# Kernel tuning notes

Measured on AMD Instinct MI355X. Metric: run time of the kernel, lower is better.

Reference implementation:

```python
import jax, jax.numpy as jnp
import numpy as np

BS, S, DIM, H = 4, 2048, 1024, 16
DH = DIM // H  # 64


def setup_inputs() -> dict:
    key = jax.random.key(0)
    ks = jax.random.split(key, 12)
    def lin(k, fan_in):
        bound = 1.0 / np.sqrt(fan_in)
        kw, kb = jax.random.split(k)
        W = jax.random.uniform(kw, (DIM, DIM), jnp.float32, -bound, bound)
        b = jax.random.uniform(kb, (DIM,), jnp.float32, -bound, bound)
        return W, b
    Wq, bq = lin(ks[0], DIM)
    Wk, bk = lin(ks[1], DIM)
    Wv, bv = lin(ks[2], DIM)
    Wo, bo = lin(ks[3], DIM)
    return {
        "query": jax.random.normal(ks[4], (BS, S, DIM), jnp.float32),
        "key": jax.random.normal(ks[5], (BS, S, DIM), jnp.float32),
        "value": jax.random.normal(ks[6], (BS, S, DIM), jnp.float32),
        "mask": jnp.ones((BS, S), jnp.int32),
        "Wq": Wq, "bq": bq, "Wk": Wk, "bk": bk,
        "Wv": Wv, "bv": bv, "Wo": Wo, "bo": bo,
    }


def reference(query, key, value, mask, Wq, bq, Wk, bk, Wv, bv, Wo, bo):
    bs, q_len, dim = query.shape
    def shape_heads(x):  # (bs, s, dim) -> (bs, H, s, DH)
        return x.reshape(bs, -1, H, DH).transpose(0, 2, 1, 3)
    # Linear projections (torch Linear: x @ W.T + b)
    q = shape_heads(query @ Wq.T + bq)
    k = shape_heads(key @ Wk.T + bk)
    v = shape_heads(value @ Wv.T + bv)
    q = q / jnp.sqrt(jnp.asarray(DH, q.dtype))
    # scores: (bs, H, q_len, k_len)
    scores = jnp.einsum('bhqd,bhkd->bhqk', q, k)
    neg = jnp.asarray(-jnp.inf, scores.dtype)
    pad = (mask == 0)[:, None, None, :]  # (bs,1,1,k_len)
    scores = jnp.where(pad, neg, scores)
    weights = jax.nn.softmax(scores, axis=-1)
    # dropout is identity in eval mode (reference is deterministic)
    context = jnp.einsum('bhqk,bhkd->bhqd', weights, v)
    context = context.transpose(0, 2, 1, 3).reshape(bs, q_len, dim)
    return context @ Wo.T + bo
```

## Files before the change

kernel.cpp:

```cpp
#include <hip/hip_runtime.h>
#include <hip/hip_bf16.h>
#include <math.h>

#define BSZ 4
#define SEQ 2048
#define DIMN 1024
#define NHEAD 16
#define DHEAD 64
#define MROWS (BSZ*SEQ)

typedef __bf16 bf16x8 __attribute__((ext_vector_type(8)));
typedef float  f32x4  __attribute__((ext_vector_type(4)));
typedef float  f32x16 __attribute__((ext_vector_type(16)));
typedef float  fvec4  __attribute__((ext_vector_type(4)));
typedef short  s16x4  __attribute__((ext_vector_type(4)));
typedef short  s16x8  __attribute__((ext_vector_type(8)));

__device__ __forceinline__ short f2bf(float v) {
  __hip_bfloat16 b = __float2bfloat16(v);
  return *reinterpret_cast<short*>(&b);
}
__device__ __forceinline__ float bf2f(short s) {
  __hip_bfloat16 b = *reinterpret_cast<__hip_bfloat16*>(&s);
  return __bfloat162float(b);
}

__device__ __forceinline__ void gld_lds16(const void* g, void* l) {
  __builtin_amdgcn_global_load_lds((const __attribute__((address_space(1))) void*)g,
                                   (__attribute__((address_space(3))) void*)l, 16, 0, 0);
}

#define QSC 0.18033688011112042f

__global__ __launch_bounds__(256) void pack_w4(
    const float* __restrict__ Wq, const float* __restrict__ Wk,
    const float* __restrict__ Wv, const float* __restrict__ Wo,
    short* __restrict__ WQh, short* __restrict__ WKh,
    short* __restrict__ WVh, short* __restrict__ WOh, short* __restrict__ WOl,
    long n)
{
  long i = ((long)blockIdx.x * 256 + threadIdx.x) * 4;
  if (i >= n) return;
  int which = blockIdx.y;
  if (which == 3) {
    fvec4 v = *(const fvec4*)&Wo[i];
    s16x4 h, l;
#pragma unroll
    for (int j = 0; j < 4; ++j) {
      short hb = f2bf(v[j]);
      h[j] = hb;
      l[j] = f2bf(v[j] - bf2f(hb));
    }
    *(s16x4*)&WOh[i] = h;
    *(s16x4*)&WOl[i] = l;
  } else {
    const float* src = which == 0 ? Wq : (which == 1 ? Wk : Wv);
    short* dst = which == 0 ? WQh : (which == 1 ? WKh : WVh);
    float sc = which == 0 ? QSC : 1.f;
    fvec4 v = *(const fvec4*)&src[i];
    s16x4 h;
#pragma unroll
    for (int j = 0; j < 4; ++j) h[j] = f2bf(v[j] * sc);
    *(s16x4*)&dst[i] = h;
  }
}

__global__ __launch_bounds__(256) void pack_hi3(
    const float* __restrict__ q, const float* __restrict__ k,
    const float* __restrict__ v,
    short* __restrict__ xq, short* __restrict__ xk, short* __restrict__ xv,
    long n)
{
  long i = ((long)blockIdx.x * 256 + threadIdx.x) * 4;
  if (i >= n) return;
  const float* src = blockIdx.y == 0 ? q : (blockIdx.y == 1 ? k : v);
  short* dst = blockIdx.y == 0 ? xq : (blockIdx.y == 1 ? xk : xv);
  fvec4 x = *(const fvec4*)&src[i];
  s16x4 h;
#pragma unroll
  for (int j = 0; j < 4; ++j) h[j] = f2bf(x[j]);
  *(s16x4*)&dst[i] = h;
}

__global__ __launch_bounds__(256) void maskbias_k(
    const int* __restrict__ mask, float* __restrict__ mb, int n)
{
  int i = blockIdx.x * 256 + threadIdx.x;
  if (i < n) mb[i] = mask[i] ? 0.f : -1e30f;
}

__global__ __launch_bounds__(64) void mask_flags(
    const int* __restrict__ mask, int* __restrict__ flg)
{
  int c = blockIdx.x;
  int base = (c >> 4) * SEQ + (c & 15) * 128;
  int m0 = mask[base + threadIdx.x];
  int m1 = mask[base + 64 + threadIdx.x];
  unsigned long long bal = __ballot(m0 != 0 && m1 != 0);
  if (threadIdx.x == 0) flg[c] = (bal == ~0ull) ? 1 : 0;
}

__global__ __launch_bounds__(256) void gemm_qkv(
    const short* __restrict__ XBq, const short* __restrict__ XBk,
    const short* __restrict__ XBv,
    const short* __restrict__ WQh, const short* __restrict__ WKh,
    const short* __restrict__ WVh,
    const float* __restrict__ bq, const float* __restrict__ bk,
    const float* __restrict__ bv,
    short* __restrict__ QB, short* __restrict__ KB, short* __restrict__ VTo)
{
  __shared__ __align__(16) short sA[128*64];
  __shared__ __align__(16) short sB[128*64];
  const int z = blockIdx.z;
  const short* A  = z == 0 ? XBq : (z == 1 ? XBk : XBv);
  const short* Bw = z == 0 ? WQh : (z == 1 ? WKh : WVh);
  const float* bias = z == 0 ? bq : (z == 1 ? bk : bv);
  short* Cb = z == 0 ? QB : (z == 1 ? KB : VTo);
  const float bscale = z == 0 ? QSC : 1.f;

  const int flat = blockIdx.y * 8 + blockIdx.x;
  const int nb = (flat & 7) * 64 + (flat >> 3);
  const int m0 = (nb >> 3) * 128, n0 = (nb & 7) * 128;

  const int t = threadIdx.x;
  const int l31 = t & 31, hi = (t >> 5) & 1, w = t >> 6;
  const int wm = w >> 1, wn = w & 1;
  const int srow7 = (t >> 3) & 7;
  const int sg = (t & 7) ^ srow7;
  int offF[4];
#pragma unroll
  for (int ks = 0; ks < 4; ++ks)
    offF[ks] = l31*64 + ((ks*2 + hi) ^ (l31 & 7))*8;

  f32x16 acc[2][2] = {};

  for (int k0 = 0; k0 < DIMN; k0 += 64) {
    __syncthreads();
#pragma unroll
    for (int i = 0; i < 4; ++i) {
      int row = i*32 + (t >> 3);
      gld_lds16(A  + (size_t)(m0+row)*DIMN + k0 + sg*8, sA + (i*256 + t)*8);
      gld_lds16(Bw + (size_t)(n0+row)*DIMN + k0 + sg*8, sB + (i*256 + t)*8);
    }
    __syncthreads();
#pragma unroll
    for (int ks = 0; ks < 4; ++ks) {
      bf16x8 af0 = *(const bf16x8*)&sA[wm*4096 + offF[ks]];
      bf16x8 af1 = *(const bf16x8*)&sA[wm*4096 + 2048 + offF[ks]];
      bf16x8 bf0 = *(const bf16x8*)&sB[wn*4096 + offF[ks]];
      bf16x8 bf1 = *(const bf16x8*)&sB[wn*4096 + 2048 + offF[ks]];
      acc[0][0] = __builtin_amdgcn_mfma_f32_32x32x16_bf16(af0, bf0, acc[0][0], 0, 0, 0);
      acc[0][1] = __builtin_amdgcn_mfma_f32_32x32x16_bf16(af0, bf1, acc[0][1], 0, 0, 0);
      acc[1][0] = __builtin_amdgcn_mfma_f32_32x32x16_bf16(af1, bf0, acc[1][0], 0, 0, 0);
      acc[1][1] = __builtin_amdgcn_mfma_f32_32x32x16_bf16(af1, bf1, acc[1][1], 0, 0, 0);
    }
  }

#pragma unroll
  for (int nt = 0; nt < 2; ++nt) {
    int col = n0 + wn*64 + nt*32 + l31;
    float bv2 = bias[col] * bscale;
    if (z == 2) {
      int hd = col >> 6, dd = col & 63;
#pragma unroll
      for (int mt = 0; mt < 2; ++mt)
#pragma unroll
        for (int rg = 0; rg < 4; ++rg) {
          int sgr = m0 + wm*64 + mt*32 + rg*8 + hi*4;
          int b = sgr >> 11, s = sgr & 2047;
          s16x4 h;
#pragma unroll
          for (int r2 = 0; r2 < 4; ++r2) h[r2] = f2bf(acc[mt][nt][rg*4+r2] + bv2);
          *(s16x4*)&Cb[((size_t)((b*16 + hd)*64 + dd))*SEQ + s] = h;
        }
    } else {
#pragma unroll
      for (int mt = 0; mt < 2; ++mt)
#pragma unroll
        for (int rg = 0; rg < 4; ++rg)
#pragma unroll
          for (int r2 = 0; r2 < 4; ++r2) {
            int row = m0 + wm*64 + mt*32 + rg*8 + hi*4 + r2;
            Cb[(size_t)row*DIMN + col] = f2bf(acc[mt][nt][rg*4+r2] + bv2);
          }
    }
  }
}

__global__ __launch_bounds__(256) void gemm_sp(
    const short* __restrict__ Ah, const short* __restrict__ Al,
    const short* __restrict__ Bh, const short* __restrict__ Bl,
    const float* __restrict__ bias, float bscale,
    float* __restrict__ C, int M, int N, int K)
{
  __shared__ __align__(16) short sA[2*128*64];
  __shared__ __align__(16) short sB[2*128*64];
  const int t = threadIdx.x;
  const int l31 = t & 31, hi = (t >> 5) & 1, w = t >> 6;
  const int wm = w >> 1, wn = w & 1;
  const int flat = blockIdx.y * 8 + blockIdx.x;
  const int nb = (flat & 7) * 64 + (flat >> 3);
  const int m0 = (nb >> 3) * 128, n0 = (nb & 7) * 128;
  const int sg = (t & 7) ^ ((t >> 3) & 7);
  int offF[4];
#pragma unroll
  for (int ks = 0; ks < 4; ++ks)
    offF[ks] = l31*64 + ((ks*2 + hi) ^ (l31 & 7))*8;

  f32x16 acc[2][2] = {};

  for (int k0 = 0; k0 < K; k0 += 64) {
    __syncthreads();
#pragma unroll
    for (int i = 0; i < 4; ++i) {
      int row = i*32 + (t >> 3);
      int u8 = (i*256 + t)*8;
      gld_lds16(Ah + (size_t)(m0+row)*K + k0 + sg*8, sA + u8);
      gld_lds16(Al + (size_t)(m0+row)*K + k0 + sg*8, sA + 8192 + u8);
      gld_lds16(Bh + (size_t)(n0+row)*K + k0 + sg*8, sB + u8);
      gld_lds16(Bl + (size_t)(n0+row)*K + k0 + sg*8, sB + 8192 + u8);
    }
    __syncthreads();
#pragma unroll
    for (int ks = 0; ks < 4; ++ks) {
      bf16x8 ah0 = *(const bf16x8*)&sA[wm*4096 + offF[ks]];
      bf16x8 ah1 = *(const bf16x8*)&sA[wm*4096 + 2048 + offF[ks]];
      bf16x8 al0 = *(const bf16x8*)&sA[8192 + wm*4096 + offF[ks]];
      bf16x8 al1 = *(const bf16x8*)&sA[8192 + wm*4096 + 2048 + offF[ks]];
      bf16x8 bh0 = *(const bf16x8*)&sB[wn*4096 + offF[ks]];
      bf16x8 bh1 = *(const bf16x8*)&sB[wn*4096 + 2048 + offF[ks]];
      bf16x8 bl0 = *(const bf16x8*)&sB[8192 + wn*4096 + offF[ks]];
      bf16x8 bl1 = *(const bf16x8*)&sB[8192 + wn*4096 + 2048 + offF[ks]];
      acc[0][0] = __builtin_amdgcn_mfma_f32_32x32x16_bf16(ah0, bh0, acc[0][0], 0, 0, 0);
      acc[0][0] = __builtin_amdgcn_mfma_f32_32x32x16_bf16(ah0, bl0, acc[0][0], 0, 0, 0);
      acc[0][0] = __builtin_amdgcn_mfma_f32_32x32x16_bf16(al0, bh0, acc[0][0], 0, 0, 0);
      acc[0][1] = __builtin_amdgcn_mfma_f32_32x32x16_bf16(ah0, bh1, acc[0][1], 0, 0, 0);
      acc[0][1] = __builtin_amdgcn_mfma_f32_32x32x16_bf16(ah0, bl1, acc[0][1], 0, 0, 0);
      acc[0][1] = __builtin_amdgcn_mfma_f32_32x32x16_bf16(al0, bh1, acc[0][1], 0, 0, 0);
      acc[1][0] = __builtin_amdgcn_mfma_f32_32x32x16_bf16(ah1, bh0, acc[1][0], 0, 0, 0);
      acc[1][0] = __builtin_amdgcn_mfma_f32_32x32x16_bf16(ah1, bl0, acc[1][0], 0, 0, 0);
      acc[1][0] = __builtin_amdgcn_mfma_f32_32x32x16_bf16(al1, bh0, acc[1][0], 0, 0, 0);
      acc[1][1] = __builtin_amdgcn_mfma_f32_32x32x16_bf16(ah1, bh1, acc[1][1], 0, 0, 0);
      acc[1][1] = __builtin_amdgcn_mfma_f32_32x32x16_bf16(ah1, bl1, acc[1][1], 0, 0, 0);
      acc[1][1] = __builtin_amdgcn_mfma_f32_32x32x16_bf16(al1, bh1, acc[1][1], 0, 0, 0);
    }
  }

#pragma unroll
  for (int nt = 0; nt < 2; ++nt) {
    int col = n0 + wn*64 + nt*32 + l31;
    float bv = bias[col] * bscale;
#pragma unroll
    for (int mt = 0; mt < 2; ++mt)
#pragma unroll
      for (int rg = 0; rg < 4; ++rg)
#pragma unroll
        for (int r2 = 0; r2 < 4; ++r2) {
          int row = m0 + wm*64 + mt*32 + rg*8 + hi*4 + r2;
          C[(size_t)row*N + col] = acc[mt][nt][rg*4+r2] + bv;
        }
  }
}

__global__ __launch_bounds__(256, 3) void attn_32(
    const short* __restrict__ QB, const short* __restrict__ KB,
    const short* __restrict__ VT, const float* __restrict__ mb,
    const int* __restrict__ flg,
    short* __restrict__ CTXh, short* __restrict__ CTXl)
{
  __shared__ __align__(16) short lds[16384];
  short* sK = lds;
  short* sV = lds + 8192;

  const int t = threadIdx.x;
  const int l31 = t & 31, hi = (t >> 5) & 1, w = t >> 6;
  const int gb = blockIdx.x;
  const int chunk = gb >> 3, qt128 = chunk & 15, bh = ((chunk >> 4) << 3) + (gb & 7);
  const int b = bh >> 4, hd = bh & 15;

#pragma unroll
  for (int i = 0; i < 4; ++i) {
    int u = i*256 + t;
    int row = u >> 3, gr = (u & 7) ^ (row & 7);
    gld_lds16(QB + ((size_t)(b*SEQ + qt128*128 + row))*DIMN + hd*64 + gr*8,
              sK + u*8);
  }
  __syncthreads();
  const int q = w*32 + l31;
  bf16x8 qf[4];
#pragma unroll
  for (int ks = 0; ks < 4; ++ks)
    qf[ks] = *(bf16x8*)&sK[q*64 + ((ks*2 + hi) ^ (q & 7))*8];

  f32x16 o_acc[2] = {};
  float m_run = -1e30f, l_run = 0.f;

  for (int kt = 0; kt < SEQ/128; ++kt) {
    __syncthreads();
#pragma unroll
    for (int i = 0; i < 4; ++i) {
      int u = i*256 + t;
      { int row = u >> 3, gr = (u & 7) ^ (row & 7);
        gld_lds16(KB + ((size_t)(b*SEQ + kt*128 + row))*DIMN + hd*64 + gr*8,
                  sK + u*8); }
      { int d = u >> 4, gr = (u & 15) ^ (d & 15);
        gld_lds16(VT + ((size_t)(bh*64 + d))*SEQ + kt*128 + gr*8,
                  sV + u*8); }
    }
    __syncthreads();

    f32x16 sacc[4] = {};
#pragma unroll
    for (int ks = 0; ks < 4; ++ks)
#pragma unroll
      for (int mt = 0; mt < 4; ++mt) {
        int kc = mt*32 + l31;
        bf16x8 kf = *(bf16x8*)&sK[kc*64 + ((ks*2 + hi) ^ (kc & 7))*8];
        sacc[mt] = __builtin_amdgcn_mfma_f32_32x32x16_bf16(kf, qf[ks], sacc[mt], 0, 0, 0);
      }

    if (!flg[b*16 + kt]) {
#pragma unroll
      for (int mt = 0; mt < 4; ++mt)
#pragma unroll
        for (int r = 0; r < 16; ++r)
          sacc[mt][r] += mb[b*SEQ + kt*128 + mt*32 + (r&3) + 8*(r>>2) + 4*hi];
    }

    float tmax = -1e30f;
#pragma unroll
    for (int mt = 0; mt < 4; ++mt)
#pragma unroll
      for (int r = 0; r < 16; ++r) tmax = fmaxf(tmax, sacc[mt][r]);
    tmax = fmaxf(tmax, __shfl_xor(tmax, 32));

    if (!__all(tmax <= m_run + 8.f)) {
      float mnew = fmaxf(m_run, tmax);
      float alpha = exp2f(m_run - mnew);
      l_run *= alpha;
#pragma unroll
      for (int dt = 0; dt < 2; ++dt)
#pragma unroll
        for (int r = 0; r < 16; ++r) o_acc[dt][r] *= alpha;
      m_run = mnew;
    }

    float rs = 0.f;
#pragma unroll
    for (int mt = 0; mt < 4; ++mt)
#pragma unroll
      for (int r = 0; r < 16; ++r) {
        float p = exp2f(sacc[mt][r] - m_run);
        sacc[mt][r] = p;
        rs += p;
      }
    rs += __shfl_xor(rs, 32);
    l_run += rs;

#pragma unroll
    for (int mt = 0; mt < 4; ++mt) {
      unsigned wv[8];
#pragma unroll
      for (int i = 0; i < 8; ++i) {
        float plo = sacc[mt][2*i], phi = sacc[mt][2*i+1];
        asm("v_cvt_pk_bf16_f32 %0, %1, %2" : "=v"(wv[i]) : "v"(plo), "v"(phi));
      }
#pragma unroll
      for (int h = 0; h < 2; ++h) {
        unsigned f0 = wv[h*4+0], f1 = wv[h*4+1], f2 = wv[h*4+2], f3 = wv[h*4+3];
        asm volatile("v_permlane32_swap_b32 %0, %1" : "+v"(f0), "+v"(f2));
        asm volatile("v_permlane32_swap_b32 %0, %1" : "+v"(f1), "+v"(f3));
        union { unsigned u[4]; bf16x8 v; } pu;
        pu.u[0] = f0; pu.u[1] = f1; pu.u[2] = f2; pu.u[3] = f3;
        const int kcs = mt*2 + h;
#pragma unroll
        for (int dt = 0; dt < 2; ++dt) {
          int d = dt*32 + l31;
          bf16x8 vf = *(bf16x8*)&sV[d*128 + ((kcs*2 + hi) ^ (d & 15))*8];
          o_acc[dt] = __builtin_amdgcn_mfma_f32_32x32x16_bf16(vf, pu.v, o_acc[dt], 0, 0, 0);
        }
      }
    }
  }

  float invl = (l_run > 0.f) ? 1.f / l_run : 0.f;
  const size_t rowbase = (size_t)(b*SEQ + qt128*128 + q)*DIMN + hd*64;
#pragma unroll
  for (int dt = 0; dt < 2; ++dt)
#pragma unroll
    for (int rg = 0; rg < 4; ++rg) {
      s16x4 hq, lq;
#pragma unroll
      for (int r2 = 0; r2 < 4; ++r2) {
        float val = o_acc[dt][rg*4 + r2] * invl;
        short hb = f2bf(val);
        hq[r2] = hb;
        lq[r2] = f2bf(val - bf2f(hb));
      }
      size_t idx = rowbase + dt*32 + rg*8 + hi*4;
      *(s16x4*)&CTXh[idx] = hq;
      *(s16x4*)&CTXl[idx] = lq;
    }
}

__global__ __launch_bounds__(256) void gemm_bt(
    const float* __restrict__ X, const float* __restrict__ W,
    const float* __restrict__ bias, float* __restrict__ C,
    int M, int N, int K)
{
  __shared__ __align__(16) float Xs[16][68];
  __shared__ __align__(16) float Ws[16][68];
  const int t  = threadIdx.x;
  const int tx = t & 15, ty = t >> 4;
  const int m0 = blockIdx.y << 6, n0 = blockIdx.x << 6;
  const int ldr = t >> 2;
  const int lk  = (t & 3) << 2;
  float acc[4][4] = {{0.f}};
  const float* Xp = X + (size_t)(m0 + ldr) * K + lk;
  const float* Wp = W + (size_t)(n0 + ldr) * K + lk;
  for (int k0 = 0; k0 < K; k0 += 16) {
    float4 xa = *(const float4*)(Xp + k0);
    float4 wa = *(const float4*)(Wp + k0);
    Xs[lk+0][ldr]=xa.x; Xs[lk+1][ldr]=xa.y; Xs[lk+2][ldr]=xa.z; Xs[lk+3][ldr]=xa.w;
    Ws[lk+0][ldr]=wa.x; Ws[lk+1][ldr]=wa.y; Ws[lk+2][ldr]=wa.z; Ws[lk+3][ldr]=wa.w;
    __syncthreads();
#pragma unroll
    for (int kk = 0; kk < 16; ++kk) {
      float4 a4 = *(const float4*)&Xs[kk][ty<<2];
      float4 b4 = *(const float4*)&Ws[kk][tx<<2];
      float av[4] = {a4.x, a4.y, a4.z, a4.w};
      float bv[4] = {b4.x, b4.y, b4.z, b4.w};
#pragma unroll
      for (int i = 0; i < 4; ++i)
#pragma unroll
        for (int j = 0; j < 4; ++j)
          acc[i][j] = fmaf(av[i], bv[j], acc[i][j]);
    }
    __syncthreads();
  }
  float4 bb4 = *(const float4*)&bias[n0 + (tx<<2)];
  const float bv[4] = {bb4.x, bb4.y, bb4.z, bb4.w};
#pragma unroll
  for (int i = 0; i < 4; ++i) {
    float4 o;
    o.x = acc[i][0]+bv[0]; o.y = acc[i][1]+bv[1];
    o.z = acc[i][2]+bv[2]; o.w = acc[i][3]+bv[3];
    *(float4*)&C[(size_t)(m0 + (ty<<2) + i) * N + n0 + (tx<<2)] = o;
  }
}

__global__ __launch_bounds__(256) void attn_fwd(
    const float* __restrict__ Q, const float* __restrict__ Kbuf,
    const float* __restrict__ Vbuf, const int* __restrict__ mask,
    float* __restrict__ CTX)
{
  __shared__ __align__(16) float Qs[64][68];
  __shared__ __align__(16) float KPs[64][68];
  __shared__ __align__(16) float Vs[64][68];
  const int t  = threadIdx.x;
  const int tx = t & 15, ty = t >> 4;
  const int qt = blockIdx.x;
  const int bh = blockIdx.y;
  const int b  = bh >> 4, h = bh & 15;
  const int ldr = t >> 2;
  const int lcb = (t & 3) << 2;
  const float* Qp = Q + (size_t)(b*SEQ + (qt<<6)) * DIMN + h*DHEAD;
#pragma unroll
  for (int u = 0; u < 4; ++u) {
    int kb = lcb + (u<<4);
    float4 q4 = *(const float4*)(Qp + (size_t)ldr*DIMN + kb);
    Qs[kb+0][ldr]=q4.x; Qs[kb+1][ldr]=q4.y; Qs[kb+2][ldr]=q4.z; Qs[kb+3][ldr]=q4.w;
  }
  float mrow[4], lsum[4], o[4][4];
#pragma unroll
  for (int i = 0; i < 4; ++i) {
    mrow[i] = -1e30f; lsum[i] = 0.f;
#pragma unroll
    for (int j = 0; j < 4; ++j) o[i][j] = 0.f;
  }
  const int qrow0 = ty << 2;
  const int col0  = tx << 2;
  for (int kt = 0; kt < SEQ/64; ++kt) {
    __syncthreads();
    const float* Kp = Kbuf + (size_t)(b*SEQ + (kt<<6)) * DIMN + h*DHEAD;
    const float* Vp = Vbuf + (size_t)(b*SEQ + (kt<<6)) * DIMN + h*DHEAD;
#pragma unroll
    for (int u = 0; u < 4; ++u) {
      int kb = lcb + (u<<4);
      float4 k4 = *(const float4*)(Kp + (size_t)ldr*DIMN + kb);
      KPs[kb+0][ldr]=k4.x; KPs[kb+1][ldr]=k4.y; KPs[kb+2][ldr]=k4.z; KPs[kb+3][ldr]=k4.w;
      float4 v4 = *(const float4*)(Vp + (size_t)ldr*DIMN + kb);
      *(float4*)&Vs[ldr][kb] = v4;
    }
    __syncthreads();
    float s[4][4] = {{0.f}};
#pragma unroll 8
    for (int kk = 0; kk < 64; ++kk) {
      float4 a4 = *(const float4*)&Qs[kk][qrow0];
      float4 b4 = *(const float4*)&KPs[kk][col0];
      float av[4] = {a4.x, a4.y, a4.z, a4.w};
      float bv[4] = {b4.x, b4.y, b4.z, b4.w};
#pragma unroll
      for (int i = 0; i < 4; ++i)
#pragma unroll
        for (int j = 0; j < 4; ++j)
          s[i][j] = fmaf(av[i], bv[j], s[i][j]);
    }
    int mk[4];
#pragma unroll
    for (int j = 0; j < 4; ++j) mk[j] = mask[b*SEQ + (kt<<6) + col0 + j];
    float p[4][4];
#pragma unroll
    for (int i = 0; i < 4; ++i) {
#pragma unroll
      for (int j = 0; j < 4; ++j)
        s[i][j] = mk[j] ? s[i][j]*0.125f : -1e30f;
      float tm = fmaxf(fmaxf(s[i][0], s[i][1]), fmaxf(s[i][2], s[i][3]));
#pragma unroll
      for (int off = 8; off >= 1; off >>= 1)
        tm = fmaxf(tm, __shfl_xor(tm, off, 64));
      float mnew  = fmaxf(mrow[i], tm);
      float aa = __expf(mrow[i] - mnew);
      mrow[i] = mnew;
      float rsum = 0.f;
#pragma unroll
      for (int j = 0; j < 4; ++j) {
        float pv = __expf(s[i][j] - mnew);
        p[i][j] = pv; rsum += pv;
      }
#pragma unroll
      for (int off = 8; off >= 1; off >>= 1)
        rsum += __shfl_xor(rsum, off, 64);
      lsum[i] = lsum[i]*aa + rsum;
#pragma unroll
      for (int j = 0; j < 4; ++j) o[i][j] *= aa;
    }
    __syncthreads();
#pragma unroll
    for (int i = 0; i < 4; ++i)
#pragma unroll
      for (int j = 0; j < 4; ++j)
        KPs[col0 + j][qrow0 + i] = p[i][j];
    __syncthreads();
#pragma unroll 8
    for (int kk = 0; kk < 64; ++kk) {
      float4 a4 = *(const float4*)&KPs[kk][qrow0];
      float4 v4 = *(const float4*)&Vs[kk][col0];
      float av[4] = {a4.x, a4.y, a4.z, a4.w};
      float vv[4] = {v4.x, v4.y, v4.z, v4.w};
#pragma unroll
      for (int i = 0; i < 4; ++i)
#pragma unroll
        for (int j = 0; j < 4; ++j)
          o[i][j] = fmaf(av[i], vv[j], o[i][j]);
    }
  }
  float* Cp = CTX + (size_t)(b*SEQ + (qt<<6)) * DIMN + h*DHEAD;
#pragma unroll
  for (int i = 0; i < 4; ++i) {
    float inv = lsum[i] > 0.f ? 1.0f/lsum[i] : 0.f;
    float4 ov;
    ov.x = o[i][0]*inv; ov.y = o[i][1]*inv;
    ov.z = o[i][2]*inv; ov.w = o[i][3]*inv;
    *(float4*)(Cp + (size_t)(qrow0 + i)*DIMN + col0) = ov;
  }
}

extern "C" void kernel_launch(void* const* d_in, const int* in_sizes, int n_in,
                              void* d_out, int out_size, void* d_ws, size_t ws_size,
                              hipStream_t stream)
{
  const float* query = (const float*)d_in[0];
  const float* key   = (const float*)d_in[1];
  const float* value = (const float*)d_in[2];
  const int*   mask  = (const int*)d_in[3];
  const float* Wq = (const float*)d_in[4];
  const float* bq = (const float*)d_in[5];
  const float* Wk = (const float*)d_in[6];
  const float* bk = (const float*)d_in[7];
  const float* Wv = (const float*)d_in[8];
  const float* bv = (const float*)d_in[9];
  const float* Wo = (const float*)d_in[10];
  const float* bo = (const float*)d_in[11];
  float* out = (float*)d_out;

  const size_t E  = (size_t)MROWS * DIMN;
  const size_t WE = (size_t)DIMN * DIMN;

  const size_t o_XB   = 5*WE*2;
  const size_t o_QB   = o_XB   + 3*E*2;
  const size_t o_KB   = o_QB   + E*2;
  const size_t o_VT   = o_KB   + E*2;
  const size_t o_CTXh = o_VT   + E*2;
  const size_t o_CTXl = o_CTXh + E*2;
  const size_t o_MB   = o_CTXl + E*2;
  const size_t o_FLG  = o_MB   + MROWS*4;
  const size_t NEED   = o_FLG  + 64*4;

  if (ws_size < NEED) {
    const size_t n = E;
    float* Qb = (float*)d_ws;
    float* Kb = Qb + n;
    float* Vb = Kb + n;
    float* Cb = Vb + n;
    dim3 gg(DIMN/64, MROWS/64), blk(256);
    hipLaunchKernelGGL(gemm_bt, gg, blk, 0, stream, query, Wq, bq, Qb, MROWS, DIMN, DIMN);
    hipLaunchKernelGGL(gemm_bt, gg, blk, 0, stream, key,   Wk, bk, Kb, MROWS, DIMN, DIMN);
    hipLaunchKernelGGL(gemm_bt, gg, blk, 0, stream, value, Wv, bv, Vb, MROWS, DIMN, DIMN);
    dim3 ga(SEQ/64, BSZ*NHEAD);
    hipLaunchKernelGGL(attn_fwd, ga, blk, 0, stream, Qb, Kb, Vb, mask, Cb);
    hipLaunchKernelGGL(gemm_bt, gg, blk, 0, stream, Cb, Wo, bo, out, MROWS, DIMN, DIMN);
    return;
  }

  char* Wp = (char*)d_ws;
  short* WQh = (short*)Wp;
  short* WKh = WQh + WE;
  short* WVh = WQh + 2*WE;
  short* WOh = WQh + 3*WE;
  short* WOl = WQh + 4*WE;
  short* XBq  = (short*)(Wp + o_XB);
  short* XBk  = XBq + E;
  short* XBv  = XBk + E;
  short* QB   = (short*)(Wp + o_QB);
  short* KB   = (short*)(Wp + o_KB);
  short* VT   = (short*)(Wp + o_VT);
  short* CTXh = (short*)(Wp + o_CTXh);
  short* CTXl = (short*)(Wp + o_CTXl);
  float* MB   = (float*)(Wp + o_MB);
  int*   FLG  = (int*)(Wp + o_FLG);

  dim3 blk(256);
  dim3 gW(WE/1024, 4), gX(E/1024, 3);
  dim3 gqkv(DIMN/128, MROWS/128, 3);
  dim3 gg(DIMN/128, MROWS/128);
  dim3 gat(BSZ*NHEAD*SEQ/128);

  hipLaunchKernelGGL(pack_w4, gW, blk, 0, stream, Wq, Wk, Wv, Wo,
                     WQh, WKh, WVh, WOh, WOl, (long)WE);
  hipLaunchKernelGGL(maskbias_k, dim3(MROWS/256), blk, 0, stream, mask, MB, MROWS);
  hipLaunchKernelGGL(mask_flags, dim3(64), dim3(64), 0, stream, mask, FLG);
  hipLaunchKernelGGL(pack_hi3, gX, blk, 0, stream, query, key, value,
                     XBq, XBk, XBv, (long)E);

  hipLaunchKernelGGL(gemm_qkv, gqkv, blk, 0, stream,
                     XBq, XBk, XBv, WQh, WKh, WVh, bq, bk, bv, QB, KB, VT);

  hipLaunchKernelGGL(attn_32, gat, blk, 0, stream, QB, KB, VT, MB, FLG, CTXh, CTXl);

  hipLaunchKernelGGL(gemm_sp, gg, blk, 0, stream, CTXh, CTXl, WOh, WOl, bo, 1.f,
                     out, MROWS, DIMN, DIMN);
}
```

Before: 399.6 us.

## Double-buffer LDS tiles in QKV projection GEMM to overlap loads with MFMA

The QKV projection GEMM now keeps two LDS buffers for the A and B tiles. It issues the direct global-to-LDS loads for the next k-step before running the MFMAs on the current buffer, then waits on vmcnt and a barrier once per iteration instead of twice. This is meant to hide global load latency behind matrix compute. In exchange, LDS use per block doubles to 64KB, which may lower occupancy.

Measured after the change: 414.8 us. +3.8%, slower.

```diff
diff --git a/kernel.cpp b/kernel.cpp
--- a/kernel.cpp
+++ b/kernel.cpp
@@ -109,8 +109,8 @@
     const float* __restrict__ bv,
     short* __restrict__ QB, short* __restrict__ KB, short* __restrict__ VTo)
 {
-  __shared__ __align__(16) short sA[128*64];
-  __shared__ __align__(16) short sB[128*64];
+  __shared__ __align__(16) short sA[2*128*64];
+  __shared__ __align__(16) short sB[2*128*64];
   const int z = blockIdx.z;
   const short* A  = z == 0 ? XBq : (z == 1 ? XBk : XBv);
   const short* Bw = z == 0 ? WQh : (z == 1 ? WKh : WVh);
@@ -125,8 +125,7 @@
   const int t = threadIdx.x;
   const int l31 = t & 31, hi = (t >> 5) & 1, w = t >> 6;
   const int wm = w >> 1, wn = w & 1;
-  const int srow7 = (t >> 3) & 7;
-  const int sg = (t & 7) ^ srow7;
+  const int sg = (t & 7) ^ ((t >> 3) & 7);
   int offF[4];
 #pragma unroll
   for (int ks = 0; ks < 4; ++ks)
@@ -134,26 +133,44 @@
 
   f32x16 acc[2][2] = {};
 
-  for (int k0 = 0; k0 < DIMN; k0 += 64) {
-    __syncthreads();
-#pragma unroll
-    for (int i = 0; i < 4; ++i) {
-      int row = i*32 + (t >> 3);
-      gld_lds16(A  + (size_t)(m0+row)*DIMN + k0 + sg*8, sA + (i*256 + t)*8);
-      gld_lds16(Bw + (size_t)(n0+row)*DIMN + k0 + sg*8, sB + (i*256 + t)*8);
-    }
-    __syncthreads();
+#pragma unroll
+  for (int i = 0; i < 4; ++i) {
+    int row = i*32 + (t >> 3);
+    gld_lds16(A  + (size_t)(m0+row)*DIMN + sg*8, sA + (i*256 + t)*8);
+    gld_lds16(Bw + (size_t)(n0+row)*DIMN + sg*8, sB + (i*256 + t)*8);
+  }
+  asm volatile("s_waitcnt vmcnt(0)" ::: "memory");
+  __builtin_amdgcn_s_barrier();
+
+  int cur = 0;
+  for (int it = 0; it < DIMN/64; ++it) {
+    if (it + 1 < DIMN/64) {
+      int k0 = (it + 1) * 64;
+      short* dA = sA + (cur ^ 1)*8192;
+      short* dB = sB + (cur ^ 1)*8192;
+#pragma unroll
+      for (int i = 0; i < 4; ++i) {
+        int row = i*32 + (t >> 3);
+        gld_lds16(A  + (size_t)(m0+row)*DIMN + k0 + sg*8, dA + (i*256 + t)*8);
+        gld_lds16(Bw + (size_t)(n0+row)*DIMN + k0 + sg*8, dB + (i*256 + t)*8);
+      }
+    }
+    const short* cA = sA + cur*8192;
+    const short* cB = sB + cur*8192;
 #pragma unroll
     for (int ks = 0; ks < 4; ++ks) {
-      bf16x8 af0 = *(const bf16x8*)&sA[wm*4096 + offF[ks]];
-      bf16x8 af1 = *(const bf16x8*)&sA[wm*4096 + 2048 + offF[ks]];
-      bf16x8 bf0 = *(const bf16x8*)&sB[wn*4096 + offF[ks]];
-      bf16x8 bf1 = *(const bf16x8*)&sB[wn*4096 + 2048 + offF[ks]];
+      bf16x8 af0 = *(const bf16x8*)&cA[wm*4096 + offF[ks]];
+      bf16x8 af1 = *(const bf16x8*)&cA[wm*4096 + 2048 + offF[ks]];
+      bf16x8 bf0 = *(const bf16x8*)&cB[wn*4096 + offF[ks]];
+      bf16x8 bf1 = *(const bf16x8*)&cB[wn*4096 + 2048 + offF[ks]];
       acc[0][0] = __builtin_amdgcn_mfma_f32_32x32x16_bf16(af0, bf0, acc[0][0], 0, 0, 0);
       acc[0][1] = __builtin_amdgcn_mfma_f32_32x32x16_bf16(af0, bf1, acc[0][1], 0, 0, 0);
       acc[1][0] = __builtin_amdgcn_mfma_f32_32x32x16_bf16(af1, bf0, acc[1][0], 0, 0, 0);
       acc[1][1] = __builtin_amdgcn_mfma_f32_32x32x16_bf16(af1, bf1, acc[1][1], 0, 0, 0);
     }
+    asm volatile("s_waitcnt vmcnt(0)" ::: "memory");
+    __builtin_amdgcn_s_barrier();
+    cur ^= 1;
   }
 
 #pragma unroll
```
